# Optimization experiments

Hardware: AMD Instinct MI355X
Metric: run time of the kernel (lower is better)

Reference implementation:

```python
import jax, jax.numpy as jnp
import numpy as np

# ---- module config (from init_kwargs) ----
KERNEL_SIZE = 3
DIM = 3
HALF = KERNEL_SIZE // 2          # kernel offsets span [-HALF, HALF]
COORD_RANGE = 256                # voxel grid extent per spatial axis
NUM_BATCH = 4
N_VOXELS = 100_000
FEAT_DIM = 32
STRIDE = COORD_RANGE + 2 * HALF  # encoding stride so shifted coords fit


def _kernel_offsets():
    # All offsets of a KERNEL_SIZE^DIM kernel, centered (MinkowskiEngine-style).
    r = np.arange(-HALF, HALF + 1)
    grids = np.meshgrid(*([r] * DIM), indexing='ij')
    return jnp.asarray(np.stack([g.ravel() for g in grids], axis=1), dtype=jnp.int32)  # [K, DIM]


def setup_inputs() -> dict:
    key = jax.random.key(0)
    k1, k2, k3 = jax.random.split(key, 3)
    batch = jax.random.randint(k1, (1, N_VOXELS), 0, NUM_BATCH, dtype=jnp.int32)
    coords = jax.random.randint(k2, (3, N_VOXELS), 0, COORD_RANGE, dtype=jnp.int32)
    sparse_indices = jnp.concatenate([batch, coords], axis=0)  # [4, N]
    features = jax.random.normal(k3, (N_VOXELS, FEAT_DIM), dtype=jnp.float32)
    return {"sparse_indices": sparse_indices, "features": features}


def _kernel_map_and_out_key(sparse_indices):
    offsets = _kernel_offsets()                 # [K, 3]
    K = offsets.shape[0]
    b = sparse_indices[0].astype(jnp.int32)     # [N]
    coords = sparse_indices[1:].T.astype(jnp.int32)  # [N, 3]
    N = coords.shape[0]
    NK = N * K

    # neighbor coords per (voxel, offset); shift by HALF so values are >= 0
    nbr = coords[:, None, :] + offsets[None, :, :] + HALF     # [N, K, 3]
    S = STRIDE
    # unique integer hash of (batch, x, y, z); fits in int32 for these ranges
    enc = ((b[:, None] * S + nbr[..., 0]) * S + nbr[..., 1]) * S + nbr[..., 2]
    enc = enc.reshape(-1)                                     # [NK]

    # unique keys (sorted) + inverse map; pad to static size NK
    uniq, inv = jnp.unique(enc, return_inverse=True, size=NK, fill_value=-1)

    # reorder unique keys into first-seen order to match the dict-based reference
    first = jnp.full((NK,), NK, dtype=jnp.int32).at[inv].min(
        jnp.arange(NK, dtype=jnp.int32))
    order = jnp.argsort(first)                                # padding sorts last
    new_id = jnp.zeros((NK,), dtype=jnp.int32).at[order].set(
        jnp.arange(NK, dtype=jnp.int32))
    out_idx = new_id[inv]                                     # [NK] output index per entry

    # decode unique (first-seen ordered) keys back to spatial coords
    uo = uniq[order]
    valid = uo >= 0
    z = uo % S
    y = (uo // S) % S
    x = (uo // (S * S)) % S
    out_key = jnp.stack([x, y, z], axis=1) - HALF             # undo shift
    out_key = jnp.where(valid[:, None], out_key, -1)          # [NK, 3], padded rows = -1

    input_idx = jnp.repeat(jnp.arange(N, dtype=jnp.int32), K) # [NK]
    rel_pos = jnp.tile(jnp.arange(K, dtype=jnp.int32), N)     # [NK]
    kernel_map = jnp.stack([input_idx, out_idx, rel_pos], axis=1)  # [NK, 3]
    return kernel_map, out_key


def reference(sparse_indices, features):
    kernel_map, out_key = _kernel_map_and_out_key(sparse_indices)
    NK = kernel_map.shape[0]
    # canonical downstream use of the kernel map: gather inputs, scatter-sum to outputs
    out_feats = jax.ops.segment_sum(features[kernel_map[:, 0]],
                                    kernel_map[:, 1], num_segments=NK)
    return kernel_map, out_key, out_feats
```

## Files before the change

### kernel.cpp

```cpp
#include <hip/hip_runtime.h>
#include <stdint.h>

typedef unsigned long long u64;
typedef unsigned u32;

#define K 27
#define S 258
#define ENCMAX (4 * S * S * S)

__global__ void k_mark(const int* __restrict__ si, int N, u64* __restrict__ bits) {
    int idx = blockIdx.x * blockDim.x + threadIdx.x;
    if (idx >= N * 9) return;
    int n = idx / 9, run = idx - n * 9;
    int ox = run / 3, oy = run - ox * 3;
    int b = si[n], x = si[N + n], y = si[2 * N + n], z = si[3 * N + n];
    unsigned enc0 = (unsigned)(((b * S + x + ox) * S + (y + oy)) * S + z);
    unsigned w = enc0 >> 6; int bit = enc0 & 63;
    atomicOr(&bits[w], 7ull << bit);
    if (bit > 61) atomicOr(&bits[w + 1], 7ull >> (64 - bit));
}

__global__ void s1_tilesum(const u64* __restrict__ bits, int* __restrict__ tsums) {
    __shared__ int s[256];
    int tid = threadIdx.x;
    const u64* p = bits + (size_t)blockIdx.x * 4096;
    int sum = 0;
    for (int j = tid; j < 4096; j += 256) sum += __popcll(p[j]);
    s[tid] = sum; __syncthreads();
    for (int off = 128; off > 0; off >>= 1) {
        if (tid < off) s[tid] += s[tid + off];
        __syncthreads();
    }
    if (tid == 0) tsums[blockIdx.x] = s[0];
}

__global__ void k_scanB(int* __restrict__ a, int n) {
    __shared__ int s[1024];
    int tid = threadIdx.x;
    int v = (tid < n) ? a[tid] : 0;
    s[tid] = v; __syncthreads();
    for (int off = 1; off < 1024; off <<= 1) {
        int t = (tid >= off) ? s[tid - off] : 0;
        __syncthreads();
        s[tid] += t;
        __syncthreads();
    }
    if (tid == 1023) a[n] = s[1023];
    if (tid < n) a[tid] = s[tid] - v;
}

__global__ void s3_wprefix(const u64* __restrict__ bits, const int* __restrict__ tsums,
                           u32* __restrict__ wprefix) {
    __shared__ int s[256];
    int tid = threadIdx.x;
    size_t base = (size_t)blockIdx.x * 4096 + (size_t)tid * 16;
    int pc[16]; int tsum = 0;
#pragma unroll
    for (int j = 0; j < 16; j++) { pc[j] = __popcll(bits[base + j]); tsum += pc[j]; }
    s[tid] = tsum; __syncthreads();
    for (int off = 1; off < 256; off <<= 1) {
        int t = (tid >= off) ? s[tid - off] : 0;
        __syncthreads();
        s[tid] += t;
        __syncthreads();
    }
    int run = tsums[blockIdx.x] + s[tid] - tsum;
#pragma unroll
    for (int j = 0; j < 16; j++) { wprefix[base + j] = (u32)run; run += pc[j]; }
}

__global__ void k_kid(const int* __restrict__ si, int N,
                      const u64* __restrict__ bits, const u32* __restrict__ wprefix,
                      int* __restrict__ kid, int* __restrict__ minE) {
    int idx = blockIdx.x * blockDim.x + threadIdx.x;
    if (idx >= N * 9) return;
    int n = idx / 9, run = idx - n * 9;
    int ox = run / 3, oy = run - ox * 3;
    int b = si[n], x = si[N + n], y = si[2 * N + n], z = si[3 * N + n];
    unsigned enc0 = (unsigned)(((b * S + x + ox) * S + (y + oy)) * S + z);
    int e0 = n * K + run * 3;
#pragma unroll
    for (int oz = 0; oz < 3; ++oz) {
        unsigned enc = enc0 + oz;
        unsigned w = enc >> 6; int bit = enc & 63;
        int kd = (int)wprefix[w] + __popcll(bits[w] & ((1ull << bit) - 1));
        kid[e0 + oz] = kd;
        atomicMin(&minE[kd], e0 + oz);
    }
}

__global__ void k_flagsum(const int* __restrict__ kid, const int* __restrict__ minE,
                          int NK, u32* __restrict__ multibk, int* __restrict__ bsums) {
    __shared__ int s[256];
    int tid = threadIdx.x;
    int base = blockIdx.x * 4096 + tid * 16;
    int kv[16];
    *(int4*)(kv + 0)  = *(const int4*)(kid + base + 0);
    *(int4*)(kv + 4)  = *(const int4*)(kid + base + 4);
    *(int4*)(kv + 8)  = *(const int4*)(kid + base + 8);
    *(int4*)(kv + 12) = *(const int4*)(kid + base + 12);
    int sum = 0;
#pragma unroll
    for (int j = 0; j < 16; j++) {
        int e = base + j;
        if (e < NK) {
            int kd = kv[j];
            if (minE[kd] == e) sum += 1;
            else atomicOr(&multibk[kd >> 5], 1u << (kd & 31));
        }
    }
    s[tid] = sum; __syncthreads();
    for (int off = 128; off > 0; off >>= 1) {
        if (tid < off) s[tid] += s[tid + off];
        __syncthreads();
    }
    if (tid == 0) bsums[blockIdx.x] = s[0];
}

__global__ void k_scanC(const int* __restrict__ kid, const int* __restrict__ minE,
                        const int* __restrict__ bsums, const int* __restrict__ si,
                        int N, int NK, float* __restrict__ out_key,
                        int* __restrict__ rank_key) {
    __shared__ int s[256];
    int tid = threadIdx.x;
    int base = blockIdx.x * 4096 + tid * 16;
    int kv[16];
    *(int4*)(kv + 0)  = *(const int4*)(kid + base + 0);
    *(int4*)(kv + 4)  = *(const int4*)(kid + base + 4);
    *(int4*)(kv + 8)  = *(const int4*)(kid + base + 8);
    *(int4*)(kv + 12) = *(const int4*)(kid + base + 12);
    int f[16]; int tsum = 0;
#pragma unroll
    for (int j = 0; j < 16; j++) {
        int e = base + j;
        f[j] = (e < NK && minE[kv[j]] == e) ? 1 : 0;
        tsum += f[j];
    }
    s[tid] = tsum; __syncthreads();
    for (int off = 1; off < 256; off <<= 1) {
        int t = (tid >= off) ? s[tid - off] : 0;
        __syncthreads();
        s[tid] += t;
        __syncthreads();
    }
    int offset = bsums[blockIdx.x] + s[tid] - tsum;
    int run = 0;
#pragma unroll
    for (int j = 0; j < 16; j++) {
        int e = base + j;
        if (f[j]) {
            int rank = offset + run;
            int n = e / K; int m = e - n * K;
            int x = si[N + n], y = si[2 * N + n], z = si[3 * N + n];
            int ox = m / 9; int rm = m - ox * 9; int oy = rm / 3; int oz = rm - oy * 3;
            out_key[(size_t)rank * 3 + 0] = (float)(x + ox - 1);
            out_key[(size_t)rank * 3 + 1] = (float)(y + oy - 1);
            out_key[(size_t)rank * 3 + 2] = (float)(z + oz - 1);
            rank_key[kv[j]] = rank;
        }
        run += f[j];
    }
}

__global__ void k_zmt(const u32* __restrict__ multibk, const int* __restrict__ rank_key,
                      const int* __restrict__ bsums, int NB, int NK, int nkw,
                      float* __restrict__ out_key, float4* __restrict__ outF4) {
    int U = bsums[NB];
    int i0 = blockIdx.x * blockDim.x + threadIdx.x;
    int gs = gridDim.x * blockDim.x;
    float4 z = {0.f, 0.f, 0.f, 0.f};
    for (int i = i0; i < nkw; i += gs) {
        u32 b = multibk[i];
        while (b) {
            int bit = __ffs(b) - 1; b &= b - 1;
            int uid = rank_key[i * 32 + bit];
            float4* q = outF4 + (size_t)uid * 8;
#pragma unroll
            for (int j = 0; j < 8; j++) q[j] = z;
        }
    }
    int rows = NK - U;
    for (int i = i0; i < rows; i += gs) {
        int row = U + i;
        float4* q = outF4 + (size_t)row * 8;
#pragma unroll
        for (int j = 0; j < 8; j++) q[j] = z;
        out_key[(size_t)row * 3 + 0] = -1.0f;
        out_key[(size_t)row * 3 + 1] = -1.0f;
        out_key[(size_t)row * 3 + 2] = -1.0f;
    }
}

__global__ void k_final(const int* __restrict__ kid, const int* __restrict__ rank_key,
                        const u32* __restrict__ multibk,
                        const float4* __restrict__ feat4,
                        float* __restrict__ km, float* __restrict__ outF, int NK) {
    int idx = blockIdx.x * blockDim.x + threadIdx.x;
    if (idx >= NK * 8) return;
    int e = idx >> 3, g = idx & 7;
    int kd = kid[e];
    int uid = rank_key[kd];
    int multi = (multibk[kd >> 5] >> (kd & 31)) & 1;
    int n = e / K, m = e - n * K;
    float4 v = feat4[(size_t)n * 8 + g];
    float* dst = outF + (size_t)uid * 32 + g * 4;
    if (multi) {
        atomicAdd(dst + 0, v.x);
        atomicAdd(dst + 1, v.y);
        atomicAdd(dst + 2, v.z);
        atomicAdd(dst + 3, v.w);
    } else {
        *(float4*)dst = v;
    }
    if (g < 3)
        km[(size_t)e * 3 + g] = (g == 0) ? (float)n
                               : ((g == 1) ? (float)uid : (float)m);
}

extern "C" void kernel_launch(void* const* d_in, const int* in_sizes, int n_in,
                              void* d_out, int out_size, void* d_ws, size_t ws_size,
                              hipStream_t stream) {
    const int* si = (const int*)d_in[0];
    const float4* feat4 = (const float4*)d_in[1];
    int N = in_sizes[0] / 4;
    int NK = N * K;
    int NKp = (NK + 4095) & ~4095;
    int NB = NKp / 4096;
    int nkw = (NK + 31) / 32;

    int NW = (ENCMAX + 63) / 64;
    int NT = (NW + 4095) / 4096;
    int NWp = NT * 4096;

    float* km = (float*)d_out;
    float* out_key = km + (size_t)NK * 3;
    float* outF = km + (size_t)NK * 6;

    char* w = (char*)d_ws;
    u64* bits     = (u64*)w; w += (size_t)NWp * 8;
    u32* wprefix  = (u32*)w; w += (size_t)NWp * 4;
    int* tsums    = (int*)w; w += (size_t)(NT + 1) * 4;
    int* minE     = (int*)w; w += (size_t)NK * 4;
    int* kid      = (int*)w; w += (size_t)NKp * 4;
    int* rank_key = (int*)w; w += (size_t)NK * 4;
    u32* multibk  = (u32*)w; w += (size_t)nkw * 4;
    int* bsums    = (int*)w;

    hipMemsetAsync(bits, 0, (size_t)NWp * 8, stream);
    hipMemsetAsync(minE, 0x7F, (size_t)NK * 4, stream);
    hipMemsetAsync(multibk, 0, (size_t)nkw * 4, stream);

    int nb9 = (N * 9 + 255) / 256;
    k_mark<<<nb9, 256, 0, stream>>>(si, N, bits);
    s1_tilesum<<<NT, 256, 0, stream>>>(bits, tsums);
    k_scanB<<<1, 1024, 0, stream>>>(tsums, NT);
    s3_wprefix<<<NT, 256, 0, stream>>>(bits, tsums, wprefix);
    k_kid<<<nb9, 256, 0, stream>>>(si, N, bits, wprefix, kid, minE);
    k_flagsum<<<NB, 256, 0, stream>>>(kid, minE, NK, multibk, bsums);
    k_scanB<<<1, 1024, 0, stream>>>(bsums, NB);
    k_scanC<<<NB, 256, 0, stream>>>(kid, minE, bsums, si, N, NK, out_key, rank_key);
    k_zmt<<<512, 256, 0, stream>>>(multibk, rank_key, bsums, NB, NK, nkw,
                                   out_key, (float4*)outF);
    k_final<<<(NK * 8 + 255) / 256, 256, 0, stream>>>(kid, rank_key, multibk,
                                                      feat4, km, outF, NK);
}
```

Measured before the change: 741.0 us.

## Fuse scans into producer kernels via last-block pattern and drop k_zmt

Each single-block scan kernel is folded into the kernel before it. The last block to finish, detected with an atomic counter, performs the scan. The minE initialization moves from a memset into s1_tilesum, and the three memsets collapse into one contiguous zeroing. Zeroing of multi-contributor output rows moves into k_scanC, which removes the k_zmt kernel. This cuts launch count and serialization points, at the cost of threadfence/atomic last-block logic and an extra multibk read per unique key.

```diff
diff --git a/kernel.cpp b/kernel.cpp
--- a/kernel.cpp
+++ b/kernel.cpp
@@ -20,33 +20,38 @@
     if (bit > 61) atomicOr(&bits[w + 1], 7ull >> (64 - bit));
 }
 
-__global__ void s1_tilesum(const u64* __restrict__ bits, int* __restrict__ tsums) {
-    __shared__ int s[256];
+__global__ void s1_tilesum(const u64* __restrict__ bits, int* __restrict__ tsums,
+                           int* __restrict__ minE, int NK, int NT,
+                           u32* __restrict__ cnt) {
+    __shared__ int s[512];
+    __shared__ int lastf;
     int tid = threadIdx.x;
     const u64* p = bits + (size_t)blockIdx.x * 4096;
     int sum = 0;
-    for (int j = tid; j < 4096; j += 256) sum += __popcll(p[j]);
+    for (int j = tid; j < 4096; j += 512) sum += __popcll(p[j]);
     s[tid] = sum; __syncthreads();
-    for (int off = 128; off > 0; off >>= 1) {
+    for (int off = 256; off > 0; off >>= 1) {
         if (tid < off) s[tid] += s[tid + off];
         __syncthreads();
     }
     if (tid == 0) tsums[blockIdx.x] = s[0];
-}
-
-__global__ void k_scanB(int* __restrict__ a, int n) {
-    __shared__ int s[1024];
-    int tid = threadIdx.x;
-    int v = (tid < n) ? a[tid] : 0;
+    for (int i = blockIdx.x * 512 + tid; i < NK; i += NT * 512)
+        minE[i] = 0x7FFFFFFF;
+    __threadfence();
+    if (tid == 0) { u32 t = atomicAdd(cnt, 1u); lastf = (t == (u32)(NT - 1)); }
+    __syncthreads();
+    if (!lastf) return;
+    __threadfence();
+    int v = (tid < NT) ? tsums[tid] : 0;
     s[tid] = v; __syncthreads();
-    for (int off = 1; off < 1024; off <<= 1) {
-        int t = (tid >= off) ? s[tid - off] : 0;
-        __syncthreads();
-        s[tid] += t;
-        __syncthreads();
-    }
-    if (tid == 1023) a[n] = s[1023];
-    if (tid < n) a[tid] = s[tid] - v;
+    for (int off = 1; off < 512; off <<= 1) {
+        int t = (tid >= off) ? s[tid - off] : 0;
+        __syncthreads();
+        s[tid] += t;
+        __syncthreads();
+    }
+    if (tid < NT) tsums[tid] = s[tid] - v;
+    if (tid == 511) tsums[NT] = s[511];
 }
 
 __global__ void s3_wprefix(const u64* __restrict__ bits, const int* __restrict__ tsums,
@@ -90,37 +95,52 @@
 }
 
 __global__ void k_flagsum(const int* __restrict__ kid, const int* __restrict__ minE,
-                          int NK, u32* __restrict__ multibk, int* __restrict__ bsums) {
-    __shared__ int s[256];
-    int tid = threadIdx.x;
-    int base = blockIdx.x * 4096 + tid * 16;
-    int kv[16];
-    *(int4*)(kv + 0)  = *(const int4*)(kid + base + 0);
-    *(int4*)(kv + 4)  = *(const int4*)(kid + base + 4);
-    *(int4*)(kv + 8)  = *(const int4*)(kid + base + 8);
-    *(int4*)(kv + 12) = *(const int4*)(kid + base + 12);
+                          int NK, int NB, u32* __restrict__ multibk,
+                          int* __restrict__ bsums, u32* __restrict__ cnt) {
+    __shared__ int s[1024];
+    __shared__ int lastf;
+    int tid = threadIdx.x;
+    int base = blockIdx.x * 4096 + tid * 4;
+    int4 kv = *(const int4*)(kid + base);
+    int kvv[4] = {kv.x, kv.y, kv.z, kv.w};
     int sum = 0;
 #pragma unroll
-    for (int j = 0; j < 16; j++) {
+    for (int j = 0; j < 4; j++) {
         int e = base + j;
         if (e < NK) {
-            int kd = kv[j];
+            int kd = kvv[j];
             if (minE[kd] == e) sum += 1;
             else atomicOr(&multibk[kd >> 5], 1u << (kd & 31));
         }
     }
     s[tid] = sum; __syncthreads();
-    for (int off = 128; off > 0; off >>= 1) {
+    for (int off = 512; off > 0; off >>= 1) {
         if (tid < off) s[tid] += s[tid + off];
         __syncthreads();
     }
     if (tid == 0) bsums[blockIdx.x] = s[0];
+    __threadfence();
+    if (tid == 0) { u32 t = atomicAdd(cnt, 1u); lastf = (t == (u32)(NB - 1)); }
+    __syncthreads();
+    if (!lastf) return;
+    __threadfence();
+    int v = (tid < NB) ? bsums[tid] : 0;
+    s[tid] = v; __syncthreads();
+    for (int off = 1; off < 1024; off <<= 1) {
+        int t = (tid >= off) ? s[tid - off] : 0;
+        __syncthreads();
+        s[tid] += t;
+        __syncthreads();
+    }
+    if (tid < NB) bsums[tid] = s[tid] - v;
+    if (tid == 1023) bsums[NB] = s[1023];
 }
 
 __global__ void k_scanC(const int* __restrict__ kid, const int* __restrict__ minE,
                         const int* __restrict__ bsums, const int* __restrict__ si,
-                        int N, int NK, float* __restrict__ out_key,
-                        int* __restrict__ rank_key) {
+                        const u32* __restrict__ multibk, int N, int NK, int NB,
+                        float* __restrict__ out_key, int* __restrict__ rank_key,
+                        float4* __restrict__ outF4) {
     __shared__ int s[256];
     int tid = threadIdx.x;
     int base = blockIdx.x * 4096 + tid * 16;
@@ -144,6 +164,7 @@
         __syncthreads();
     }
     int offset = bsums[blockIdx.x] + s[tid] - tsum;
+    float4 zf = {0.f, 0.f, 0.f, 0.f};
     int run = 0;
 #pragma unroll
     for (int j = 0; j < 16; j++) {
@@ -156,35 +177,24 @@
             out_key[(size_t)rank * 3 + 0] = (float)(x + ox - 1);
             out_key[(size_t)rank * 3 + 1] = (float)(y + oy - 1);
             out_key[(size_t)rank * 3 + 2] = (float)(z + oz - 1);
-            rank_key[kv[j]] = rank;
+            int kd = kv[j];
+            rank_key[kd] = rank;
+            if ((multibk[kd >> 5] >> (kd & 31)) & 1) {
+                float4* q = outF4 + (size_t)rank * 8;
+#pragma unroll
+                for (int q8 = 0; q8 < 8; q8++) q[q8] = zf;
+            }
         }
         run += f[j];
     }
-}
-
-__global__ void k_zmt(const u32* __restrict__ multibk, const int* __restrict__ rank_key,
-                      const int* __restrict__ bsums, int NB, int NK, int nkw,
-                      float* __restrict__ out_key, float4* __restrict__ outF4) {
     int U = bsums[NB];
-    int i0 = blockIdx.x * blockDim.x + threadIdx.x;
+    int rows = NK - U;
     int gs = gridDim.x * blockDim.x;
-    float4 z = {0.f, 0.f, 0.f, 0.f};
-    for (int i = i0; i < nkw; i += gs) {
-        u32 b = multibk[i];
-        while (b) {
-            int bit = __ffs(b) - 1; b &= b - 1;
-            int uid = rank_key[i * 32 + bit];
-            float4* q = outF4 + (size_t)uid * 8;
-#pragma unroll
-            for (int j = 0; j < 8; j++) q[j] = z;
-        }
-    }
-    int rows = NK - U;
-    for (int i = i0; i < rows; i += gs) {
+    for (int i = blockIdx.x * blockDim.x + tid; i < rows; i += gs) {
         int row = U + i;
         float4* q = outF4 + (size_t)row * 8;
 #pragma unroll
-        for (int j = 0; j < 8; j++) q[j] = z;
+        for (int q8 = 0; q8 < 8; q8++) q[q8] = zf;
         out_key[(size_t)row * 3 + 0] = -1.0f;
         out_key[(size_t)row * 3 + 1] = -1.0f;
         out_key[(size_t)row * 3 + 2] = -1.0f;
@@ -237,30 +247,37 @@
     float* outF = km + (size_t)NK * 6;
 
     char* w = (char*)d_ws;
-    u64* bits     = (u64*)w; w += (size_t)NWp * 8;
-    u32* wprefix  = (u32*)w; w += (size_t)NWp * 4;
-    int* tsums    = (int*)w; w += (size_t)(NT + 1) * 4;
-    int* minE     = (int*)w; w += (size_t)NK * 4;
-    int* kid      = (int*)w; w += (size_t)NKp * 4;
-    int* rank_key = (int*)w; w += (size_t)NK * 4;
-    u32* multibk  = (u32*)w; w += (size_t)nkw * 4;
-    int* bsums    = (int*)w;
-
-    hipMemsetAsync(bits, 0, (size_t)NWp * 8, stream);
-    hipMemsetAsync(minE, 0x7F, (size_t)NK * 4, stream);
-    hipMemsetAsync(multibk, 0, (size_t)nkw * 4, stream);
+    char* p_bits    = w; w += ((size_t)NWp * 8 + 15) & ~(size_t)15;
+    char* p_multibk = w; w += ((size_t)nkw * 4 + 15) & ~(size_t)15;
+    char* p_cnts    = w; w += 16;
+    size_t zbytes   = (size_t)(w - (char*)d_ws);
+    char* p_tsums   = w; w += ((size_t)(NT + 1) * 4 + 15) & ~(size_t)15;
+    char* p_wpref   = w; w += ((size_t)NWp * 4 + 15) & ~(size_t)15;
+    char* p_minE    = w; w += ((size_t)NK * 4 + 15) & ~(size_t)15;
+    char* p_kid     = w; w += ((size_t)NKp * 4 + 15) & ~(size_t)15;
+    char* p_rank    = w; w += ((size_t)NK * 4 + 15) & ~(size_t)15;
+    char* p_bsums   = w; w += ((size_t)(NB + 1) * 4 + 15) & ~(size_t)15;
+
+    u64* bits     = (u64*)p_bits;
+    u32* multibk  = (u32*)p_multibk;
+    u32* cnts     = (u32*)p_cnts;
+    int* tsums    = (int*)p_tsums;
+    u32* wprefix  = (u32*)p_wpref;
+    int* minE     = (int*)p_minE;
+    int* kid      = (int*)p_kid;
+    int* rank_key = (int*)p_rank;
+    int* bsums    = (int*)p_bsums;
+
+    hipMemsetAsync(d_ws, 0, zbytes, stream);
 
     int nb9 = (N * 9 + 255) / 256;
     k_mark<<<nb9, 256, 0, stream>>>(si, N, bits);
-    s1_tilesum<<<NT, 256, 0, stream>>>(bits, tsums);
-    k_scanB<<<1, 1024, 0, stream>>>(tsums, NT);
+    s1_tilesum<<<NT, 512, 0, stream>>>(bits, tsums, minE, NK, NT, cnts);
     s3_wprefix<<<NT, 256, 0, stream>>>(bits, tsums, wprefix);
     k_kid<<<nb9, 256, 0, stream>>>(si, N, bits, wprefix, kid, minE);
-    k_flagsum<<<NB, 256, 0, stream>>>(kid, minE, NK, multibk, bsums);
-    k_scanB<<<1, 1024, 0, stream>>>(bsums, NB);
-    k_scanC<<<NB, 256, 0, stream>>>(kid, minE, bsums, si, N, NK, out_key, rank_key);
-    k_zmt<<<512, 256, 0, stream>>>(multibk, rank_key, bsums, NB, NK, nkw,
-                                   out_key, (float4*)outF);
+    k_flagsum<<<NB, 1024, 0, stream>>>(kid, minE, NK, NB, multibk, bsums, cnts + 1);
+    k_scanC<<<NB, 256, 0, stream>>>(kid, minE, bsums, si, multibk, N, NK, NB,
+                                    out_key, rank_key, (float4*)outF);
     k_final<<<(NK * 8 + 255) / 256, 256, 0, stream>>>(kid, rank_key, multibk,
                                                       feat4, km, outF, NK);
 }
```

New measurement: 961.6 us. 29.8% more time.
